# Kernel tuning notes

Measured on AMD Instinct MI355X. Metric: run time of the kernel, lower is better.

## Reference

```python
import jax, jax.numpy as jnp
import numpy as np

TAU = 2.0        # MultiStepLIFNode tau
ALPHA = 4.0      # sigmoid surrogate-gradient sharpness (spikingjelly default)
BN_EPS = 1e-5

@jax.custom_vjp
def heaviside(x):
    return (x >= 0.0).astype(x.dtype)

def _h_fwd(x):
    return (x >= 0.0).astype(x.dtype), x

def _h_bwd(res, g):
    s = jax.nn.sigmoid(ALPHA * res)
    return (g * ALPHA * s * (1.0 - s),)

heaviside.defvjp(_h_fwd, _h_bwd)

def lif(x_seq, v_threshold=1.0):
    """Multi-step LIF, hard reset to 0, decay_input, detach_reset. x_seq: [T, ...]"""
    def step(v, x):
        v = v + (x - v) / TAU
        spike = heaviside(v - v_threshold)
        v = v * (1.0 - jax.lax.stop_gradient(spike))
        return v, spike
    _, spikes = jax.lax.scan(step, jnp.zeros_like(x_seq[0]), x_seq)
    return spikes

def conv1x1_bn(x, w, gamma, beta, mean, var, bias=None):
    # x: [T,B,C,H,W]; 1x1 conv == channel matmul; BN in eval mode (affine fold)
    y = jnp.einsum('tbchw,oc->tbohw', x, w)
    if bias is not None:
        y = y + bias[None, None, :, None, None]
    inv = gamma / jnp.sqrt(var + BN_EPS)
    return y * inv[None, None, :, None, None] + (beta - mean * inv)[None, None, :, None, None]

def setup_inputs() -> dict:
    key = jax.random.key(0)
    T, B, C, H, W = 4, 16, 512, 32, 32
    ks = jax.random.split(key, 18)
    def w(k):
        return jax.random.normal(k, (C, C), jnp.float32) * (1.0 / np.sqrt(C))
    def vec_n(k):
        return jax.random.normal(k, (C,), jnp.float32) * 0.1
    def vec_p(k):
        return jax.random.uniform(k, (C,), jnp.float32, 0.5, 1.5)
    return {
        'x': jax.random.normal(ks[0], (T, B, C, H, W), jnp.float32),
        'q_w': w(ks[1]), 'q_gamma': vec_p(ks[2]), 'q_beta': vec_n(ks[3]),
        'q_mean': vec_n(ks[4]), 'q_var': vec_p(ks[5]),
        'k_w': w(ks[6]), 'k_gamma': vec_p(ks[7]), 'k_beta': vec_n(ks[8]),
        'k_mean': vec_n(ks[9]), 'k_var': vec_p(ks[10]),
        'proj_w': w(ks[11]), 'proj_b': vec_n(ks[12]), 'proj_gamma': vec_p(ks[13]),
        'proj_beta': vec_n(ks[14]), 'proj_mean': vec_n(ks[15]), 'proj_var': vec_p(ks[16]),
        'num_heads': 8,
    }

def reference(x, q_w, q_gamma, q_beta, q_mean, q_var,
              k_w, k_gamma, k_beta, k_mean, k_var,
              proj_w, proj_b, proj_gamma, proj_beta, proj_mean, proj_var,
              num_heads):
    T, B, C, H, W = x.shape
    hd = C // num_heads
    # Q / K branches: conv1x1 -> BN -> LIF spikes
    q = lif(conv1x1_bn(x, q_w, q_gamma, q_beta, q_mean, q_var))          # [T,B,C,H,W]
    k = lif(conv1x1_bn(x, k_w, k_gamma, k_beta, k_mean, k_var))          # [T,B,C,H,W]
    # sum over head-channel dim (keepdim), spike-gate at threshold 0.5
    q = q.reshape(T, B, num_heads, hd, H, W).sum(axis=3, keepdims=True)  # [T,B,nh,1,H,W]
    attn = lif(q, v_threshold=0.5)                                       # [T,B,nh,1,H,W]
    # elementwise gated attention (broadcast over head channels)
    y = (attn * k.reshape(T, B, num_heads, hd, H, W)).reshape(T, B, C, H, W)
    # projection: conv1x1(+bias) -> BN -> LIF
    y = lif(conv1x1_bn(y, proj_w, proj_gamma, proj_beta, proj_mean, proj_var, bias=proj_b))
    return y
```

## Files before the change

kernel.cpp:

```cpp
#include <hip/hip_runtime.h>
#include <cstdint>
#include <math.h>

#define TT 4
#define BB 16
#define CCH 512
#define HWD 1024
#define NHH 8
#define NW 16
#define MQK 1.5e-4
#define MPROJ 1.0e-4
#define CAPQ 49152
#define CAPP 16384
#define WTSZ 262144
#define XSOFF 12345600ULL
#define XSBYTES 134217728ULL
#define WSNEED (XSOFF + XSBYTES)

typedef __attribute__((ext_vector_type(4))) float f32x4;
typedef __attribute__((ext_vector_type(8))) short s16x8;
typedef __attribute__((ext_vector_type(4))) uint32_t u32x4;

static __device__ __forceinline__ f32x4 MFMA(s16x8 a, s16x8 b, f32x4 c) {
    return __builtin_amdgcn_mfma_f32_16x16x32_bf16(a, b, c, 0, 0, 0);
}

static __device__ __forceinline__ uint32_t hi_pair(uint32_t u0, uint32_t u1) {
#if __has_builtin(__builtin_amdgcn_perm)
    return __builtin_amdgcn_perm(u1, u0, 0x07060302u);
#else
    return (u1 & 0xFFFF0000u) | (u0 >> 16);
#endif
}
static __device__ __forceinline__ uint32_t lo_pair(uint32_t u0, uint32_t u1) {
#if __has_builtin(__builtin_amdgcn_perm)
    return __builtin_amdgcn_perm(u1, u0, 0x05040100u);
#else
    return ((u1 & 0xFFFFu) << 16) | (u0 & 0xFFFFu);
#endif
}

struct SplitPair { uint32_t h, l; };

static __device__ __forceinline__ SplitPair split_pair(float f0, float f1) {
    const uint32_t u0 = __builtin_bit_cast(uint32_t, f0);
    const uint32_t u1 = __builtin_bit_cast(uint32_t, f1);
    SplitPair r;
    r.h = hi_pair(u0, u1);
    const float r0 = f0 - __builtin_bit_cast(float, u0 & 0xFFFF0000u);
    const float r1 = f1 - __builtin_bit_cast(float, u1 & 0xFFFF0000u);
    r.l = hi_pair(__builtin_bit_cast(uint32_t, r0), __builtin_bit_cast(uint32_t, r1));
    return r;
}

static __device__ __forceinline__ void load_split_frag(const float* p, s16x8& h, s16x8& l) {
    const float4 a = *(const float4*)p;
    const float4 b4 = *(const float4*)(p + 4);
    u32x4 hw_, lw_;
    const SplitPair p0 = split_pair(a.x, a.y);
    const SplitPair p1 = split_pair(a.z, a.w);
    const SplitPair p2 = split_pair(b4.x, b4.y);
    const SplitPair p3 = split_pair(b4.z, b4.w);
    hw_[0] = p0.h; lw_[0] = p0.l;
    hw_[1] = p1.h; lw_[1] = p1.l;
    hw_[2] = p2.h; lw_[2] = p2.l;
    hw_[3] = p3.h; lw_[3] = p3.l;
    h = __builtin_bit_cast(s16x8, hw_);
    l = __builtin_bit_cast(s16x8, lw_);
}

static __device__ __forceinline__ uint32_t packsplit(float f) {
    const uint32_t u = __builtin_bit_cast(uint32_t, f);
    const uint32_t hi = u & 0xFFFF0000u;
    const float r = f - __builtin_bit_cast(float, hi);
    return hi | (__builtin_bit_cast(uint32_t, r) >> 16);
}

static __device__ __forceinline__ void probe_bf16(int lane, int rowD[4], int colD[4],
                                                  int& aRow, int& aKb, int& bCol, int& bKb)
{
    const f32x4 z = {0.f, 0.f, 0.f, 0.f};
    const short lv = (short)(__builtin_bit_cast(uint32_t, (float)lane) >> 16);
    const short one = (short)0x3F80;
    const s16x8 av = {lv, lv, lv, lv, lv, lv, lv, lv};
    const s16x8 ov = {one, one, one, one, one, one, one, one};
    const f32x4 pa = MFMA(av, ov, z);
    const f32x4 pb = MFMA(ov, av, z);
    bool A2 = false, B2 = false;
#pragma unroll
    for (int r = 0; r < 4; ++r) {
        const int va = (int)pa[r];
        if (((va - 48) & 127) == 0) { rowD[r] = (va - 48) >> 7; A2 = true; }
        else                        { rowD[r] = (va - 768) >> 5; }
        const int vb = (int)pb[r];
        if (((vb - 48) & 127) == 0) { colD[r] = (vb - 48) >> 7; B2 = true; }
        else                        { colD[r] = (vb - 768) >> 5; }
    }
    aRow = A2 ? (lane >> 2) : (lane & 15);
    aKb  = A2 ? (lane & 3) * 8 : (lane >> 4) * 8;
    bCol = B2 ? (lane >> 2) : (lane & 15);
    bKb  = B2 ? (lane & 3) * 8 : (lane >> 4) * 8;
}

__global__ void k_zero(unsigned int* ctr) {
    if (threadIdx.x < 2) ctr[threadIdx.x] = 0u;
}

__global__ __launch_bounds__(256) void k_xsplit(const float* __restrict__ x,
                                                uint32_t* __restrict__ xs)
{
    const size_t N = (size_t)TT * BB * CCH * HWD;
    size_t i = ((size_t)blockIdx.x * 256 + threadIdx.x) * 4;
    const size_t stride = (size_t)gridDim.x * 1024;
    for (; i < N; i += stride) {
        const float4 v = *(const float4*)&x[i];
        u32x4 p;
        p[0] = packsplit(v.x); p[1] = packsplit(v.y);
        p[2] = packsplit(v.z); p[3] = packsplit(v.w);
        *(u32x4*)&xs[i] = p;
    }
}

__global__ __launch_bounds__(256) void k_prep(
    const float* __restrict__ qw, const float* __restrict__ kw, const float* __restrict__ pw,
    const float* __restrict__ qg, const float* __restrict__ qbe,
    const float* __restrict__ qm, const float* __restrict__ qva,
    const float* __restrict__ kg, const float* __restrict__ kbe,
    const float* __restrict__ km, const float* __restrict__ kva,
    const float* __restrict__ pg, const float* __restrict__ pbe,
    const float* __restrict__ pm, const float* __restrict__ pva,
    const float* __restrict__ pb,
    unsigned short* __restrict__ wt, double* __restrict__ bnc)
{
    const int bx = blockIdx.x;
    const int mat = bx >> 5, ot = bx & 31;
    const float* W = (mat == 0) ? qw : ((mat == 1) ? kw : pw);
    unsigned short* hi = wt + (size_t)(mat * 2 + 0) * WTSZ;
    unsigned short* lo = wt + (size_t)(mat * 2 + 1) * WTSZ;
#pragma unroll
    for (int it = 0; it < 4; ++it) {
        const int j = it * 256 + threadIdx.x;
        const int ks = j >> 6, sub = j & 63;
        const int kgrp = sub >> 4, row = sub & 15;
        const float* src = W + (size_t)(ot * 16 + row) * CCH + ks * 32 + kgrp * 8;
        s16x8 h, l;
        load_split_frag(src, h, l);
        *(s16x8*)&hi[((size_t)(ot * 16 + ks) * 64 + sub) * 8] = h;
        *(s16x8*)&lo[((size_t)(ot * 16 + ks) * 64 + sub) * 8] = l;
    }
    if (ot == 0) {
        const float* g  = (mat == 0) ? qg  : ((mat == 1) ? kg  : pg);
        const float* be = (mat == 0) ? qbe : ((mat == 1) ? kbe : pbe);
        const float* mn = (mat == 0) ? qm  : ((mat == 1) ? km  : pm);
        const float* va = (mat == 0) ? qva : ((mat == 1) ? kva : pva);
        for (int o = threadIdx.x; o < CCH; o += 256) {
            const double inv = (double)g[o] / sqrt((double)va[o] + 1e-5);
            double add = (double)be[o] - (double)mn[o] * inv;
            if (mat == 2) add = add + (double)pb[o] * inv;
            bnc[(size_t)(mat * CCH + o) * 2]     = inv;
            bnc[(size_t)(mat * CCH + o) * 2 + 1] = add;
        }
    }
}

template<bool PRE>
__global__ __launch_bounds__(256, 2) void k_qk(
    const float* __restrict__ x, const uint32_t* __restrict__ xsp,
    const unsigned short* __restrict__ wt, const double* __restrict__ bnc,
    uint32_t* __restrict__ qbits, uint32_t* __restrict__ kbits,
    unsigned int* __restrict__ ctr, uint32_t* __restrict__ list)
{
    __shared__ uint32_t Xs[2][8192];
    __shared__ uint32_t QB[2][2][TT][64];

    const int tid = threadIdx.x, lane = tid & 63, wid = tid >> 6;
    const int b   = blockIdx.z;
    const int o0  = blockIdx.y * 64, hw0 = blockIdx.x * 64;
    const int worow = (wid >> 1) * 32, whw = (wid & 1) * 32;

    int rowD[4], colD[4], aRow, aKb, bCol, bKb;
    probe_bf16(lane, rowD, colD, aRow, aKb, bCol, bKb);

    const int laneoff = ((aKb >> 3) * 16 + aRow) * 8;
    const int kgrp = bKb >> 3;
    const int roff0 = (whw + 0  + bCol) ^ (kgrp << 4);
    const int roff1 = (whw + 16 + bCol) ^ (kgrp << 4);
    const int otg0 = blockIdx.y * 4 + (wid >> 1) * 2;

    int sDst[8];
    uint32_t sOff[8];
#pragma unroll
    for (int it = 0; it < 8; ++it) {
        const int j = it * 256 + tid;
        const int t = j >> 9, c = (j >> 4) & 31, hw4 = j & 15;
        sDst[it] = (t * 32 + c) * 64 + ((hw4 * 4) ^ (((c >> 3) & 3) << 4));
        sOff[it] = (uint32_t)(((t * BB + b) * CCH + c) * HWD + hw0 + hw4 * 4);
    }

    f32x4 aq[TT][2][2], ak[TT][2][2];
#pragma unroll
    for (int t = 0; t < TT; ++t)
#pragma unroll
        for (int ot = 0; ot < 2; ++ot)
#pragma unroll
            for (int ht = 0; ht < 2; ++ht) {
                aq[t][ot][ht] = (f32x4){0.f, 0.f, 0.f, 0.f};
                ak[t][ot][ht] = (f32x4){0.f, 0.f, 0.f, 0.f};
            }

    u32x4 st[8];
    auto loadch = [&](int ks) {
#pragma unroll
        for (int it = 0; it < 8; ++it) {
            const size_t off = (size_t)sOff[it] + (size_t)ks * 32 * HWD;
            if constexpr (PRE) {
                st[it] = *(const u32x4*)&xsp[off];
            } else {
                const float4 v = *(const float4*)&x[off];
                u32x4 p;
                p[0] = packsplit(v.x); p[1] = packsplit(v.y);
                p[2] = packsplit(v.z); p[3] = packsplit(v.w);
                st[it] = p;
            }
        }
    };

    loadch(0);
#pragma unroll
    for (int it = 0; it < 8; ++it) *(u32x4*)&Xs[0][sDst[it]] = st[it];
    __syncthreads();

    int cur = 0;
#pragma unroll 1
    for (int ks = 0; ks < 16; ++ks) {
        if (ks < 15) loadch(ks + 1);

        s16x8 Aqh[2], Aql[2], Akh[2], Akl[2];
#pragma unroll
        for (int ot = 0; ot < 2; ++ot) {
            const size_t tb = ((size_t)(otg0 + ot) * 16 + ks) * 512 + laneoff;
            Aqh[ot] = *(const s16x8*)&wt[0 * WTSZ + tb];
            Aql[ot] = *(const s16x8*)&wt[1 * WTSZ + tb];
            Akh[ot] = *(const s16x8*)&wt[2 * WTSZ + tb];
            Akl[ot] = *(const s16x8*)&wt[3 * WTSZ + tb];
        }

        const uint32_t* Bb = Xs[cur];
#pragma unroll
        for (int t = 0; t < TT; ++t) {
            const uint32_t* Bp = Bb + t * 2048 + kgrp * 512;
            uint32_t w[8];
#pragma unroll
            for (int e = 0; e < 8; ++e) w[e] = Bp[e * 64 + roff0];
            u32x4 bh, bl;
            bh[0] = hi_pair(w[0], w[1]); bl[0] = lo_pair(w[0], w[1]);
            bh[1] = hi_pair(w[2], w[3]); bl[1] = lo_pair(w[2], w[3]);
            bh[2] = hi_pair(w[4], w[5]); bl[2] = lo_pair(w[4], w[5]);
            bh[3] = hi_pair(w[6], w[7]); bl[3] = lo_pair(w[6], w[7]);
            const s16x8 Bh0 = __builtin_bit_cast(s16x8, bh);
            const s16x8 Bl0 = __builtin_bit_cast(s16x8, bl);
#pragma unroll
            for (int e = 0; e < 8; ++e) w[e] = Bp[e * 64 + roff1];
            bh[0] = hi_pair(w[0], w[1]); bl[0] = lo_pair(w[0], w[1]);
            bh[1] = hi_pair(w[2], w[3]); bl[1] = lo_pair(w[2], w[3]);
            bh[2] = hi_pair(w[4], w[5]); bl[2] = lo_pair(w[4], w[5]);
            bh[3] = hi_pair(w[6], w[7]); bl[3] = lo_pair(w[6], w[7]);
            const s16x8 Bh1 = __builtin_bit_cast(s16x8, bh);
            const s16x8 Bl1 = __builtin_bit_cast(s16x8, bl);
#pragma unroll
            for (int ot = 0; ot < 2; ++ot) {
                aq[t][ot][0] = MFMA(Aqh[ot], Bh0, aq[t][ot][0]);
                aq[t][ot][0] = MFMA(Aqh[ot], Bl0, aq[t][ot][0]);
                aq[t][ot][0] = MFMA(Aql[ot], Bh0, aq[t][ot][0]);
                ak[t][ot][0] = MFMA(Akh[ot], Bh0, ak[t][ot][0]);
                ak[t][ot][0] = MFMA(Akh[ot], Bl0, ak[t][ot][0]);
                ak[t][ot][0] = MFMA(Akl[ot], Bh0, ak[t][ot][0]);
                aq[t][ot][1] = MFMA(Aqh[ot], Bh1, aq[t][ot][1]);
                aq[t][ot][1] = MFMA(Aqh[ot], Bl1, aq[t][ot][1]);
                aq[t][ot][1] = MFMA(Aql[ot], Bh1, aq[t][ot][1]);
                ak[t][ot][1] = MFMA(Akh[ot], Bh1, ak[t][ot][1]);
                ak[t][ot][1] = MFMA(Akh[ot], Bl1, ak[t][ot][1]);
                ak[t][ot][1] = MFMA(Akl[ot], Bh1, ak[t][ot][1]);
            }
        }

        if (ks < 15) {
#pragma unroll
            for (int it = 0; it < 8; ++it) *(u32x4*)&Xs[cur ^ 1][sDst[it]] = st[it];
        }
        __syncthreads();
        cur ^= 1;
    }

#pragma unroll
    for (int u = 0; u < 8; ++u) ((uint32_t*)QB)[tid + u * 256] = 0u;
    __syncthreads();

    auto chains = [&](f32x4 (&acc)[TT][2][2], int br) {
#pragma unroll
        for (int ot = 0; ot < 2; ++ot)
#pragma unroll
            for (int ht = 0; ht < 2; ++ht)
#pragma unroll
                for (int r = 0; r < 4; ++r) {
                    const int orow = worow + ot * 16 + rowD[r];
                    const int o = o0 + orow;
                    const double inv = bnc[(size_t)(br * CCH + o) * 2];
                    const double add = bnc[(size_t)(br * CCH + o) * 2 + 1];
                    const uint32_t bit = 1u << (orow & 31);
                    const int ow = orow >> 5;
                    const int hwq = whw + ht * 16 + colD[r];
                    double v = 0.0; bool fl = false;
#pragma unroll
                    for (int t = 0; t < TT; ++t) {
                        const double y = (double)acc[t][ot][ht][r] * inv + add;
                        v = v + (y - v) * 0.5;
                        if (fabs(v - 1.0) < MQK) fl = true;
                        if (v >= 1.0) { atomicOr(&QB[br][ow][t][hwq], bit); v = 0.0; }
                    }
                    if (fl) {
                        const unsigned int idx = atomicAdd(ctr, 1u);
                        if (idx < CAPQ)
                            list[idx] = (uint32_t)((br << 23) | (o << 14) | (b << 10) | (hw0 + hwq));
                    }
                }
    };
    chains(aq, 0);
    chains(ak, 1);
    __syncthreads();

#pragma unroll
    for (int u = 0; u < 4; ++u) {
        const int idx = tid + u * 256;
        const int br = idx >> 9, ow = (idx >> 8) & 1, t = (idx >> 6) & 3, hwq = idx & 63;
        uint32_t* dst = br ? kbits : qbits;
        dst[((size_t)(t * BB + b) * NW + (o0 >> 5) + ow) * HWD + hw0 + hwq] = QB[br][ow][t][hwq];
    }
}

__global__ __launch_bounds__(256) void k_fix_qk(
    const float* __restrict__ x,
    const float* __restrict__ qw, const float* __restrict__ qg, const float* __restrict__ qbe,
    const float* __restrict__ qm, const float* __restrict__ qva,
    const float* __restrict__ kw, const float* __restrict__ kg, const float* __restrict__ kbe,
    const float* __restrict__ km, const float* __restrict__ kva,
    const unsigned int* __restrict__ ctr, const uint32_t* __restrict__ list,
    uint32_t* __restrict__ qbits, uint32_t* __restrict__ kbits)
{
    const int lane = threadIdx.x & 63;
    const int wg = (blockIdx.x * blockDim.x + threadIdx.x) >> 6;
    const int nw = (gridDim.x * blockDim.x) >> 6;
    unsigned int n = *ctr; if (n > CAPQ) n = CAPQ;

    for (unsigned int i = wg; i < n; i += nw) {
        const uint32_t e = list[i];
        const int br = (e >> 23) & 1, o = (e >> 14) & 511, b = (e >> 10) & 15, hw = e & 1023;
        const float* w = (br ? kw : qw) + (size_t)o * CCH;
        double dots[TT];
#pragma unroll
        for (int t = 0; t < TT; ++t) {
            double s = 0.0;
            for (int c = lane; c < CCH; c += 64)
                s += (double)w[c] * (double)x[((size_t)(t * BB + b) * CCH + c) * HWD + hw];
#pragma unroll
            for (int off = 32; off; off >>= 1) s += __shfl_xor(s, off);
            dots[t] = s;
        }
        if (lane == 0) {
            const float* g  = br ? kg  : qg;
            const float* be = br ? kbe : qbe;
            const float* mn = br ? km  : qm;
            const float* va = br ? kva : qva;
            const double inv = (double)g[o] / sqrt((double)va[o] + 1e-5);
            const double add = (double)be[o] - (double)mn[o] * inv;
            uint32_t* bits = br ? kbits : qbits;
            double v = 0.0;
#pragma unroll
            for (int t = 0; t < TT; ++t) {
                const double y = dots[t] * inv + add;
                v = v + (y - v) * 0.5;
                const size_t wa = ((size_t)(t * BB + b) * NW + (o >> 5)) * HWD + hw;
                const uint32_t bit = 1u << (o & 31);
                if (v >= 1.0) { atomicOr(&bits[wa], bit); v = 0.0; }
                else          { atomicAnd(&bits[wa], ~bit); }
            }
        }
    }
}

__global__ __launch_bounds__(256) void k_attn(
    const uint32_t* __restrict__ qbits, uint8_t* __restrict__ attn)
{
    const int idx = blockIdx.x * 256 + threadIdx.x;
    const int hw = idx & (HWD - 1);
    const int h  = (idx >> 10) & (NHH - 1);
    const int b  = idx >> 13;
    double v = 0.0;
#pragma unroll
    for (int t = 0; t < TT; ++t) {
        const uint32_t w0 = qbits[((size_t)(t * BB + b) * NW + h * 2    ) * HWD + hw];
        const uint32_t w1 = qbits[((size_t)(t * BB + b) * NW + h * 2 + 1) * HWD + hw];
        const double q = (double)(__popc(w0) + __popc(w1));
        v = v + (q - v) * 0.5;
        const uint8_t s = (v >= 0.5) ? (uint8_t)1 : (uint8_t)0;
        attn[((size_t)(t * BB + b) * NHH + h) * HWD + hw] = s;
        if (s) v = 0.0;
    }
}

__global__ __launch_bounds__(256) void k_proj(
    const unsigned short* __restrict__ wt, const double* __restrict__ bnc,
    const uint32_t* __restrict__ kbits, const uint8_t* __restrict__ attn,
    float* __restrict__ out,
    unsigned int* __restrict__ ctr2, uint32_t* __restrict__ list2)
{
    const int tid = threadIdx.x, lane = tid & 63, wid = tid >> 6;
    const int b   = blockIdx.z;
    const int o0  = blockIdx.y * 128, hw0 = blockIdx.x * 32;
    const int worow = (wid >> 1) * 64, whw = (wid & 1) * 16;

    int rowD[4], colD[4], aRow, aKb, bCol, bKb;
    probe_bf16(lane, rowD, colD, aRow, aKb, bCol, bKb);
    const int laneoff = ((aKb >> 3) * 16 + aRow) * 8;
    const int hwB = hw0 + whw + bCol;
    const int otg0 = blockIdx.y * 8 + (wid >> 1) * 4;

    f32x4 acc[TT][4];
#pragma unroll
    for (int t = 0; t < TT; ++t)
#pragma unroll
        for (int ot = 0; ot < 4; ++ot) acc[t][ot] = (f32x4){0.f, 0.f, 0.f, 0.f};

#pragma unroll 1
    for (int ks = 0; ks < 16; ++ks) {
        s16x8 Ah[4], Al[4];
#pragma unroll
        for (int ot = 0; ot < 4; ++ot) {
            const size_t tb = ((size_t)(otg0 + ot) * 16 + ks) * 512 + laneoff;
            Ah[ot] = *(const s16x8*)&wt[4 * WTSZ + tb];
            Al[ot] = *(const s16x8*)&wt[5 * WTSZ + tb];
        }
#pragma unroll
        for (int t = 0; t < TT; ++t) {
            const size_t tb = (size_t)(t * BB + b);
            const uint32_t kv = kbits[(tb * NW + ks) * HWD + hwB];
            const uint32_t av = attn[(tb * NHH + (ks >> 1)) * HWD + hwB];
            const uint32_t mask = av ? kv : 0u;
            const uint32_t byt = (mask >> bKb) & 0xFFu;
            u32x4 bw;
#pragma unroll
            for (int j = 0; j < 4; ++j)
                bw[j] = (((byt >> (2 * j)) & 1u) ? 0x3F80u : 0u)
                      | (((byt >> (2 * j + 1)) & 1u) ? 0x3F800000u : 0u);
            const s16x8 By = __builtin_bit_cast(s16x8, bw);
#pragma unroll
            for (int ot = 0; ot < 4; ++ot) {
                acc[t][ot] = MFMA(Ah[ot], By, acc[t][ot]);
                acc[t][ot] = MFMA(Al[ot], By, acc[t][ot]);
            }
        }
    }

#pragma unroll
    for (int ot = 0; ot < 4; ++ot)
#pragma unroll
        for (int r = 0; r < 4; ++r) {
            const int o = o0 + worow + ot * 16 + rowD[r];
            const int hwD = hw0 + whw + colD[r];
            const double inv = bnc[(size_t)(2 * CCH + o) * 2];
            const double add = bnc[(size_t)(2 * CCH + o) * 2 + 1];
            double v = 0.0; bool fl = false;
#pragma unroll
            for (int t = 0; t < TT; ++t) {
                const double y = (double)acc[t][ot][r] * inv + add;
                v = v + (y - v) * 0.5;
                if (fabs(v - 1.0) < MPROJ) fl = true;
                float s;
                if (v >= 1.0) { s = 1.0f; v = 0.0; } else { s = 0.0f; }
                out[((size_t)(t * BB + b) * CCH + o) * HWD + hwD] = s;
            }
            if (fl) {
                const unsigned int idx = atomicAdd(ctr2, 1u);
                if (idx < CAPP) list2[idx] = (uint32_t)((o << 14) | (b << 10) | hwD);
            }
        }
}

__global__ __launch_bounds__(256) void k_fix_proj(
    const float* __restrict__ pw, const float* __restrict__ pb,
    const float* __restrict__ pg, const float* __restrict__ pbe,
    const float* __restrict__ pm, const float* __restrict__ pva,
    const uint32_t* __restrict__ kbits, const uint8_t* __restrict__ attn,
    const unsigned int* __restrict__ ctr2, const uint32_t* __restrict__ list2,
    float* __restrict__ out)
{
    const int lane = threadIdx.x & 63;
    const int wg = (blockIdx.x * blockDim.x + threadIdx.x) >> 6;
    const int nw = (gridDim.x * blockDim.x) >> 6;
    unsigned int n = *ctr2; if (n > CAPP) n = CAPP;

    for (unsigned int i = wg; i < n; i += nw) {
        const uint32_t e = list2[i];
        const int o = (e >> 14) & 511, b = (e >> 10) & 15, hw = e & 1023;
        const float* w = pw + (size_t)o * CCH;
        double dots[TT];
#pragma unroll
        for (int t = 0; t < TT; ++t) {
            double s = 0.0;
            for (int c = lane; c < CCH; c += 64) {
                const uint32_t kv = kbits[((size_t)(t * BB + b) * NW + (c >> 5)) * HWD + hw];
                const uint32_t av = attn[((size_t)(t * BB + b) * NHH + (c >> 6)) * HWD + hw];
                if (av && ((kv >> (c & 31)) & 1u)) s += (double)w[c];
            }
#pragma unroll
            for (int off = 32; off; off >>= 1) s += __shfl_xor(s, off);
            dots[t] = s;
        }
        if (lane == 0) {
            const double inv = (double)pg[o] / sqrt((double)pva[o] + 1e-5);
            const double add = (double)pbe[o] - (double)pm[o] * inv;
            const double bias = (double)pb[o];
            double v = 0.0;
#pragma unroll
            for (int t = 0; t < TT; ++t) {
                const double y = (dots[t] + bias) * inv + add;
                v = v + (y - v) * 0.5;
                float s;
                if (v >= 1.0) { s = 1.0f; v = 0.0; } else { s = 0.0f; }
                out[((size_t)(t * BB + b) * CCH + o) * HWD + hw] = s;
            }
        }
    }
}

extern "C" void kernel_launch(void* const* d_in, const int* in_sizes, int n_in,
                              void* d_out, int out_size, void* d_ws, size_t ws_size,
                              hipStream_t stream)
{
    (void)in_sizes; (void)n_in; (void)out_size;

    const float* x   = (const float*)d_in[0];
    const float* qw  = (const float*)d_in[1];
    const float* qg  = (const float*)d_in[2];
    const float* qbe = (const float*)d_in[3];
    const float* qm  = (const float*)d_in[4];
    const float* qv  = (const float*)d_in[5];
    const float* kw  = (const float*)d_in[6];
    const float* kg  = (const float*)d_in[7];
    const float* kbe = (const float*)d_in[8];
    const float* km  = (const float*)d_in[9];
    const float* kv  = (const float*)d_in[10];
    const float* pw  = (const float*)d_in[11];
    const float* pb  = (const float*)d_in[12];
    const float* pg  = (const float*)d_in[13];
    const float* pbe = (const float*)d_in[14];
    const float* pm  = (const float*)d_in[15];
    const float* pv  = (const float*)d_in[16];

    uint8_t* base = (uint8_t*)d_ws;
    uint32_t* qbits = (uint32_t*)base;
    uint32_t* kbits = (uint32_t*)(base + 4194304);
    uint8_t*  attn  = base + 8388608;
    unsigned int* ctr = (unsigned int*)(base + 8912896);
    uint32_t* qklist  = (uint32_t*)(base + 8913152);
    uint32_t* prlist  = (uint32_t*)(base + 9109760);
    unsigned short* wtiles = (unsigned short*)(base + 9175296);
    double* bnc = (double*)(base + 12321024);
    uint32_t* xsp = (uint32_t*)(base + XSOFF);
    float* out = (float*)d_out;

    const bool pre = ws_size >= WSNEED;

    k_zero<<<1, 64, 0, stream>>>(ctr);
    k_prep<<<96, 256, 0, stream>>>(qw, kw, pw, qg, qbe, qm, qv,
                                   kg, kbe, km, kv, pg, pbe, pm, pv, pb,
                                   wtiles, bnc);
    if (pre) {
        k_xsplit<<<2048, 256, 0, stream>>>(x, xsp);
        k_qk<true><<<dim3(HWD / 64, CCH / 64, BB), 256, 0, stream>>>(
            x, xsp, wtiles, bnc, qbits, kbits, ctr, qklist);
    } else {
        k_qk<false><<<dim3(HWD / 64, CCH / 64, BB), 256, 0, stream>>>(
            x, xsp, wtiles, bnc, qbits, kbits, ctr, qklist);
    }
    k_fix_qk<<<256, 256, 0, stream>>>(x, qw, qg, qbe, qm, qv,
                                      kw, kg, kbe, km, kv, ctr, qklist, qbits, kbits);
    k_attn<<<(BB * NHH * HWD) / 256, 256, 0, stream>>>(qbits, attn);
    k_proj<<<dim3(HWD / 32, CCH / 128, BB), 256, 0, stream>>>(
        wtiles, bnc, kbits, attn, out, ctr + 1, prlist);
    k_fix_proj<<<64, 256, 0, stream>>>(pw, pb, pg, pbe, pm, pv,
                                       kbits, attn, ctr + 1, prlist, out);
}
```

Measured before the change: 463.8 us.

## Drop x pre-split pass and split QK tile across 8 waves per block

```diff
diff --git a/kernel.cpp b/kernel.cpp
--- a/kernel.cpp
+++ b/kernel.cpp
@@ -13,9 +13,6 @@
 #define CAPQ 49152
 #define CAPP 16384
 #define WTSZ 262144
-#define XSOFF 12345600ULL
-#define XSBYTES 134217728ULL
-#define WSNEED (XSOFF + XSBYTES)
 
 typedef __attribute__((ext_vector_type(4))) float f32x4;
 typedef __attribute__((ext_vector_type(8))) short s16x8;
@@ -106,21 +103,6 @@
     if (threadIdx.x < 2) ctr[threadIdx.x] = 0u;
 }
 
-__global__ __launch_bounds__(256) void k_xsplit(const float* __restrict__ x,
-                                                uint32_t* __restrict__ xs)
-{
-    const size_t N = (size_t)TT * BB * CCH * HWD;
-    size_t i = ((size_t)blockIdx.x * 256 + threadIdx.x) * 4;
-    const size_t stride = (size_t)gridDim.x * 1024;
-    for (; i < N; i += stride) {
-        const float4 v = *(const float4*)&x[i];
-        u32x4 p;
-        p[0] = packsplit(v.x); p[1] = packsplit(v.y);
-        p[2] = packsplit(v.z); p[3] = packsplit(v.w);
-        *(u32x4*)&xs[i] = p;
-    }
-}
-
 __global__ __launch_bounds__(256) void k_prep(
     const float* __restrict__ qw, const float* __restrict__ kw, const float* __restrict__ pw,
     const float* __restrict__ qg, const float* __restrict__ qbe,
@@ -163,9 +145,8 @@
     }
 }
 
-template<bool PRE>
-__global__ __launch_bounds__(256, 2) void k_qk(
-    const float* __restrict__ x, const uint32_t* __restrict__ xsp,
+__global__ __launch_bounds__(512, 4) void k_qk(
+    const float* __restrict__ x,
     const unsigned short* __restrict__ wt, const double* __restrict__ bnc,
     uint32_t* __restrict__ qbits, uint32_t* __restrict__ kbits,
     unsigned int* __restrict__ ctr, uint32_t* __restrict__ list)
@@ -176,7 +157,7 @@
     const int tid = threadIdx.x, lane = tid & 63, wid = tid >> 6;
     const int b   = blockIdx.z;
     const int o0  = blockIdx.y * 64, hw0 = blockIdx.x * 64;
-    const int worow = (wid >> 1) * 32, whw = (wid & 1) * 32;
+    const int worow = (wid >> 1) * 16, whw = (wid & 1) * 32;
 
     int rowD[4], colD[4], aRow, aKb, bCol, bKb;
     probe_bf16(lane, rowD, colD, aRow, aKb, bCol, bKb);
@@ -185,49 +166,42 @@
     const int kgrp = bKb >> 3;
     const int roff0 = (whw + 0  + bCol) ^ (kgrp << 4);
     const int roff1 = (whw + 16 + bCol) ^ (kgrp << 4);
-    const int otg0 = blockIdx.y * 4 + (wid >> 1) * 2;
-
-    int sDst[8];
-    uint32_t sOff[8];
-#pragma unroll
-    for (int it = 0; it < 8; ++it) {
-        const int j = it * 256 + tid;
+    const int otg = blockIdx.y * 4 + (wid >> 1);
+
+    int sDst[4];
+    uint32_t sOff[4];
+#pragma unroll
+    for (int it = 0; it < 4; ++it) {
+        const int j = it * 512 + tid;
         const int t = j >> 9, c = (j >> 4) & 31, hw4 = j & 15;
         sDst[it] = (t * 32 + c) * 64 + ((hw4 * 4) ^ (((c >> 3) & 3) << 4));
         sOff[it] = (uint32_t)(((t * BB + b) * CCH + c) * HWD + hw0 + hw4 * 4);
     }
 
-    f32x4 aq[TT][2][2], ak[TT][2][2];
+    f32x4 aq[TT][2], ak[TT][2];
 #pragma unroll
     for (int t = 0; t < TT; ++t)
 #pragma unroll
-        for (int ot = 0; ot < 2; ++ot)
-#pragma unroll
-            for (int ht = 0; ht < 2; ++ht) {
-                aq[t][ot][ht] = (f32x4){0.f, 0.f, 0.f, 0.f};
-                ak[t][ot][ht] = (f32x4){0.f, 0.f, 0.f, 0.f};
-            }
-
-    u32x4 st[8];
+        for (int ht = 0; ht < 2; ++ht) {
+            aq[t][ht] = (f32x4){0.f, 0.f, 0.f, 0.f};
+            ak[t][ht] = (f32x4){0.f, 0.f, 0.f, 0.f};
+        }
+
+    u32x4 st[4];
     auto loadch = [&](int ks) {
 #pragma unroll
-        for (int it = 0; it < 8; ++it) {
-            const size_t off = (size_t)sOff[it] + (size_t)ks * 32 * HWD;
-            if constexpr (PRE) {
-                st[it] = *(const u32x4*)&xsp[off];
-            } else {
-                const float4 v = *(const float4*)&x[off];
-                u32x4 p;
-                p[0] = packsplit(v.x); p[1] = packsplit(v.y);
-                p[2] = packsplit(v.z); p[3] = packsplit(v.w);
-                st[it] = p;
-            }
+        for (int it = 0; it < 4; ++it) {
+            const float4 v = *(const float4*)&x[(size_t)sOff[it] + (size_t)ks * 32 * HWD];
+            u32x4 p;
+            p[0] = packsplit(v.x); p[1] = packsplit(v.y);
+            p[2] = packsplit(v.z); p[3] = packsplit(v.w);
+            st[it] = p;
         }
     };
 
     loadch(0);
 #pragma unroll
-    for (int it = 0; it < 8; ++it) *(u32x4*)&Xs[0][sDst[it]] = st[it];
+    for (int it = 0; it < 4; ++it) *(u32x4*)&Xs[0][sDst[it]] = st[it];
     __syncthreads();
 
     int cur = 0;
@@ -235,15 +209,11 @@
     for (int ks = 0; ks < 16; ++ks) {
         if (ks < 15) loadch(ks + 1);
 
-        s16x8 Aqh[2], Aql[2], Akh[2], Akl[2];
-#pragma unroll
-        for (int ot = 0; ot < 2; ++ot) {
-            const size_t tb = ((size_t)(otg0 + ot) * 16 + ks) * 512 + laneoff;
-            Aqh[ot] = *(const s16x8*)&wt[0 * WTSZ + tb];
-            Aql[ot] = *(const s16x8*)&wt[1 * WTSZ + tb];
-            Akh[ot] = *(const s16x8*)&wt[2 * WTSZ + tb];
-            Akl[ot] = *(const s16x8*)&wt[3 * WTSZ + tb];
-        }
+        const size_t tb = ((size_t)otg * 16 + ks) * 512 + laneoff;
+        const s16x8 Aqh = *(const s16x8*)&wt[0 * WTSZ + tb];
+        const s16x8 Aql = *(const s16x8*)&wt[1 * WTSZ + tb];
+        const s16x8 Akh = *(const s16x8*)&wt[2 * WTSZ + tb];
+        const s16x8 Akl = *(const s16x8*)&wt[3 * WTSZ + tb];
 
         const uint32_t* Bb = Xs[cur];
 #pragma unroll
@@ -267,71 +237,67 @@
             bh[3] = hi_pair(w[6], w[7]); bl[3] = lo_pair(w[6], w[7]);
             const s16x8 Bh1 = __builtin_bit_cast(s16x8, bh);
             const s16x8 Bl1 = __builtin_bit_cast(s16x8, bl);
-#pragma unroll
-            for (int ot = 0; ot < 2; ++ot) {
-                aq[t][ot][0] = MFMA(Aqh[ot], Bh0, aq[t][ot][0]);
-                aq[t][ot][0] = MFMA(Aqh[ot], Bl0, aq[t][ot][0]);
-                aq[t][ot][0] = MFMA(Aql[ot], Bh0, aq[t][ot][0]);
-                ak[t][ot][0] = MFMA(Akh[ot], Bh0, ak[t][ot][0]);
-                ak[t][ot][0] = MFMA(Akh[ot], Bl0, ak[t][ot][0]);
-                ak[t][ot][0] = MFMA(Akl[ot], Bh0, ak[t][ot][0]);
-                aq[t][ot][1] = MFMA(Aqh[ot], Bh1, aq[t][ot][1]);
-                aq[t][ot][1] = MFMA(Aqh[ot], Bl1, aq[t][ot][1]);
-                aq[t][ot][1] = MFMA(Aql[ot], Bh1, aq[t][ot][1]);
-                ak[t][ot][1] = MFMA(Akh[ot], Bh1, ak[t][ot][1]);
-                ak[t][ot][1] = MFMA(Akh[ot], Bl1, ak[t][ot][1]);
-                ak[t][ot][1] = MFMA(Akl[ot], Bh1, ak[t][ot][1]);
-            }
+
+            aq[t][0] = MFMA(Aqh, Bh0, aq[t][0]);
+            aq[t][0] = MFMA(Aqh, Bl0, aq[t][0]);
+            aq[t][0] = MFMA(Aql, Bh0, aq[t][0]);
+            ak[t][0] = MFMA(Akh, Bh0, ak[t][0]);
+            ak[t][0] = MFMA(Akh, Bl0, ak[t][0]);
+            ak[t][0] = MFMA(Akl, Bh0, ak[t][0]);
+            aq[t][1] = MFMA(Aqh, Bh1, aq[t][1]);
+            aq[t][1] = MFMA(Aqh, Bl1, aq[t][1]);
+            aq[t][1] = MFMA(Aql, Bh1, aq[t][1]);
+            ak[t][1] = MFMA(Akh, Bh1, ak[t][1]);
+            ak[t][1] = MFMA(Akh, Bl1, ak[t][1]);
+            ak[t][1] = MFMA(Akl, Bh1, ak[t][1]);
         }
 
         if (ks < 15) {
 #pragma unroll
-            for (int it = 0; it < 8; ++it) *(u32x4*)&Xs[cur ^ 1][sDst[it]] = st[it];
+            for (int it = 0; it < 4; ++it) *(u32x4*)&Xs[cur ^ 1][sDst[it]] = st[it];
         }
         __syncthreads();
         cur ^= 1;
     }
 
 #pragma unroll
-    for (int u = 0; u < 8; ++u) ((uint32_t*)QB)[tid + u * 256] = 0u;
+    for (int u = 0; u < 2; ++u) ((uint32_t*)QB)[tid + u * 512] = 0u;
     __syncthreads();
 
-    auto chains = [&](f32x4 (&acc)[TT][2][2], int br) {
-#pragma unroll
-        for (int ot = 0; ot < 2; ++ot)
-#pragma unroll
-            for (int ht = 0; ht < 2; ++ht)
-#pragma unroll
-                for (int r = 0; r < 4; ++r) {
-                    const int orow = worow + ot * 16 + rowD[r];
-                    const int o = o0 + orow;
-                    const double inv = bnc[(size_t)(br * CCH + o) * 2];
-                    const double add = bnc[(size_t)(br * CCH + o) * 2 + 1];
-                    const uint32_t bit = 1u << (orow & 31);
-                    const int ow = orow >> 5;
-                    const int hwq = whw + ht * 16 + colD[r];
-                    double v = 0.0; bool fl = false;
-#pragma unroll
-                    for (int t = 0; t < TT; ++t) {
-                        const double y = (double)acc[t][ot][ht][r] * inv + add;
-                        v = v + (y - v) * 0.5;
-                        if (fabs(v - 1.0) < MQK) fl = true;
-                        if (v >= 1.0) { atomicOr(&QB[br][ow][t][hwq], bit); v = 0.0; }
-                    }
-                    if (fl) {
-                        const unsigned int idx = atomicAdd(ctr, 1u);
-                        if (idx < CAPQ)
-                            list[idx] = (uint32_t)((br << 23) | (o << 14) | (b << 10) | (hw0 + hwq));
-                    }
+    auto chains = [&](f32x4 (&acc)[TT][2], int br) {
+#pragma unroll
+        for (int ht = 0; ht < 2; ++ht)
+#pragma unroll
+            for (int r = 0; r < 4; ++r) {
+                const int orow = worow + rowD[r];
+                const int o = o0 + orow;
+                const double inv = bnc[(size_t)(br * CCH + o) * 2];
+                const double add = bnc[(size_t)(br * CCH + o) * 2 + 1];
+                const uint32_t bit = 1u << (orow & 31);
+                const int ow = orow >> 5;
+                const int hwq = whw + ht * 16 + colD[r];
+                double v = 0.0; bool fl = false;
+#pragma unroll
+                for (int t = 0; t < TT; ++t) {
+                    const double y = (double)acc[t][ht][r] * inv + add;
+                    v = v + (y - v) * 0.5;
+                    if (fabs(v - 1.0) < MQK) fl = true;
+                    if (v >= 1.0) { atomicOr(&QB[br][ow][t][hwq], bit); v = 0.0; }
                 }
+                if (fl) {
+                    const unsigned int idx = atomicAdd(ctr, 1u);
+                    if (idx < CAPQ)
+                        list[idx] = (uint32_t)((br << 23) | (o << 14) | (b << 10) | (hw0 + hwq));
+                }
+            }
     };
     chains(aq, 0);
     chains(ak, 1);
     __syncthreads();
 
 #pragma unroll
-    for (int u = 0; u < 4; ++u) {
-        const int idx = tid + u * 256;
+    for (int u = 0; u < 2; ++u) {
+        const int idx = tid + u * 512;
         const int br = idx >> 9, ow = (idx >> 8) & 1, t = (idx >> 6) & 3, hwq = idx & 63;
         uint32_t* dst = br ? kbits : qbits;
         dst[((size_t)(t * BB + b) * NW + (o0 >> 5) + ow) * HWD + hw0 + hwq] = QB[br][ow][t][hwq];
@@ -537,7 +503,7 @@
                               void* d_out, int out_size, void* d_ws, size_t ws_size,
                               hipStream_t stream)
 {
-    (void)in_sizes; (void)n_in; (void)out_size;
+    (void)in_sizes; (void)n_in; (void)out_size; (void)ws_size;
 
     const float* x   = (const float*)d_in[0];
     const float* qw  = (const float*)d_in[1];
@@ -566,23 +532,14 @@
     uint32_t* prlist  = (uint32_t*)(base + 9109760);
     unsigned short* wtiles = (unsigned short*)(base + 9175296);
     double* bnc = (double*)(base + 12321024);
-    uint32_t* xsp = (uint32_t*)(base + XSOFF);
     float* out = (float*)d_out;
-
-    const bool pre = ws_size >= WSNEED;
 
     k_zero<<<1, 64, 0, stream>>>(ctr);
     k_prep<<<96, 256, 0, stream>>>(qw, kw, pw, qg, qbe, qm, qv,
                                    kg, kbe, km, kv, pg, pbe, pm, pv, pb,
                                    wtiles, bnc);
-    if (pre) {
-        k_xsplit<<<2048, 256, 0, stream>>>(x, xsp);
-        k_qk<true><<<dim3(HWD / 64, CCH / 64, BB), 256, 0, stream>>>(
-            x, xsp, wtiles, bnc, qbits, kbits, ctr, qklist);
-    } else {
-        k_qk<false><<<dim3(HWD / 64, CCH / 64, BB), 256, 0, stream>>>(
-            x, xsp, wtiles, bnc, qbits, kbits, ctr, qklist);
-    }
+    k_qk<<<dim3(HWD / 64, CCH / 64, BB), 512, 0, stream>>>(
+        x, wtiles, bnc, qbits, kbits, ctr, qklist);
     k_fix_qk<<<256, 256, 0, stream>>>(x, qw, qg, qbe, qm, qv,
                                       kw, kg, kbe, km, kv, ctr, qklist, qbits, kbits);
     k_attn<<<(BB * NHH * HWD) / 256, 256, 0, stream>>>(qbits, attn);
```

Result: no change. 470.8 us (+1.5%).
